# Kernel tuning notes

Hardware: AMD Instinct MI355X
Metric: run time of the kernel (lower is better)

The kernel has to match this reference:

```python
import jax, jax.numpy as jnp
import numpy as np

N_NODES = 100000
N_EDGES = 1600000
IN_DIM, HID_DIM, OUT_DIM = 128, 128, 64


def gcn_conv(x, W, b, src, dst, edge_weight, n_nodes):
    """PyG GCNConv: symmetric norm with self-loops (weight 1.0), x@W, scatter-add, +bias."""
    xw = x @ W                                   # [N, out]
    deg = jax.ops.segment_sum(edge_weight, dst, num_segments=n_nodes) + 1.0  # self-loop weight 1
    dis = jnp.where(deg > 0, jax.lax.rsqrt(deg), 0.0)       # deg^{-1/2}
    norm = dis[src] * edge_weight * dis[dst]                # per-edge norm
    agg = jax.ops.segment_sum(norm[:, None] * xw[src], dst, num_segments=n_nodes)
    self_term = (dis * dis)[:, None] * xw                   # self-loop contribution
    return agg + self_term + b


def setup_inputs() -> dict:
    key = jax.random.key(0)
    ks = jax.random.split(key, 12)
    x = jax.random.normal(ks[0], (N_NODES, IN_DIM), dtype=jnp.float32)
    edge_index = jax.random.randint(ks[1], (2, N_EDGES), 0, N_NODES, dtype=jnp.int64 if jax.config.jax_enable_x64 else jnp.int32)
    edge_curvature = jax.random.normal(ks[2], (N_EDGES, 1), dtype=jnp.float32)
    s = 0.1
    W1 = jax.random.normal(ks[3], (IN_DIM, HID_DIM), dtype=jnp.float32) * s
    b1 = jnp.zeros((HID_DIM,), dtype=jnp.float32)
    W2 = jax.random.normal(ks[4], (HID_DIM, OUT_DIM), dtype=jnp.float32) * s
    b2 = jnp.zeros((OUT_DIM,), dtype=jnp.float32)
    mw1 = jax.random.normal(ks[5], (1, 16), dtype=jnp.float32) * s
    mb1 = jnp.zeros((16,), dtype=jnp.float32)
    mw2 = jax.random.normal(ks[6], (16, 1), dtype=jnp.float32) * s
    mb2 = jnp.zeros((1,), dtype=jnp.float32)
    return {"x": x, "edge_index": edge_index, "edge_curvature": edge_curvature,
            "W1": W1, "b1": b1, "W2": W2, "b2": b2,
            "mw1": mw1, "mb1": mb1, "mw2": mw2, "mb2": mb2}


def reference(x, edge_index, edge_curvature, W1, b1, W2, b2, mw1, mb1, mw2, mb2):
    src, dst = edge_index[0], edge_index[1]
    # curv_mlp: Linear(1,16) -> ReLU -> Linear(16,1) -> Sigmoid
    h = jax.nn.relu(edge_curvature @ mw1 + mb1)
    w = jax.nn.sigmoid(h @ mw2 + mb2)[:, 0]
    edge_weight = 0.1 + 0.9 * w
    h1 = jax.nn.relu(gcn_conv(x, W1, b1, src, dst, edge_weight, N_NODES))
    # dropout p=0.5 is identity in eval mode
    out = gcn_conv(h1, W2, b2, src, dst, edge_weight, N_NODES)
    return out
```

## Files before the change

### kernel.cpp

```cpp
#include <hip/hip_runtime.h>


constexpr int N_NODES = 100000;
constexpr int N_EDGES = 1600000;
constexpr int IN_DIM  = 128;
constexpr int HID_DIM = 128;
constexpr int OUT_DIM = 64;

constexpr int RANGE = 256;
constexpr int NBUK  = (N_NODES + RANGE - 1) / RANGE;
constexpr int EPB   = 4096;
constexpr int NPART = (N_EDGES + EPB - 1) / EPB;

using bf16x8 = __attribute__((ext_vector_type(8))) short;
using f32x4  = __attribute__((ext_vector_type(4))) float;

__device__ __forceinline__ unsigned short f2b(float f)
{
    unsigned int u = __float_as_uint(f);
    u += 0x7fffu + ((u >> 16) & 1u);
    return (unsigned short)(u >> 16);
}

__device__ __forceinline__ float edge_weight_mlp(float c,
                                                 const float* __restrict__ mw1,
                                                 const float* __restrict__ mb1,
                                                 const float* __restrict__ mw2,
                                                 const float* __restrict__ mb2)
{
    float z = mb2[0];
#pragma unroll
    for (int i = 0; i < 16; ++i) {
        float h = fmaf(c, mw1[i], mb1[i]);
        h = fmaxf(h, 0.0f);
        z = fmaf(h, mw2[i], z);
    }
    float s = 1.0f / (1.0f + __expf(-z));
    return fmaf(0.9f, s, 0.1f);
}

__global__ __launch_bounds__(512) void k_hist(const int* __restrict__ dst,
                                              int* __restrict__ blockHist,
                                              int* __restrict__ gcnt)
{
    __shared__ int hist[NBUK];
    const int tid = threadIdx.x;
    for (int i = tid; i < NBUK; i += 512) hist[i] = 0;
    __syncthreads();
    const int base = blockIdx.x * EPB;
    const int n = min(EPB, N_EDGES - base);
    for (int i = tid; i < n; i += 512)
        atomicAdd(&hist[dst[base + i] >> 8], 1);
    __syncthreads();
    for (int i = tid; i < NBUK; i += 512) {
        int h = hist[i];
        blockHist[(size_t)blockIdx.x * NBUK + i] = h;
        if (h) atomicAdd(&gcnt[i], h);
    }
}

__global__ __launch_bounds__(512) void k_scan_buckets(const int* __restrict__ gcnt,
                                                      int* __restrict__ bucketBase)
{
    __shared__ int sm[512];
    const int t = threadIdx.x;
    int v = (t < NBUK) ? gcnt[t] : 0;
    sm[t] = v;
    __syncthreads();
#pragma unroll
    for (int o = 1; o < 512; o <<= 1) {
        int u = (t >= o) ? sm[t - o] : 0;
        __syncthreads();
        sm[t] += u;
        __syncthreads();
    }
    if (t < NBUK) bucketBase[t] = sm[t] - v;
    if (t == NBUK - 1) bucketBase[NBUK] = sm[t];
}

__global__ __launch_bounds__(256) void k_colscan(int* __restrict__ blockHist,
                                                 const int* __restrict__ bucketBase)
{
    int j = blockIdx.x * blockDim.x + threadIdx.x;
    if (j >= NBUK) return;
    int run = bucketBase[j];
    for (int b = 0; b < NPART; ++b) {
        size_t idx = (size_t)b * NBUK + j;
        int t = blockHist[idx];
        blockHist[idx] = run;
        run += t;
    }
}

__global__ __launch_bounds__(512) void k_partition(const float* __restrict__ curv,
                                                   const int*   __restrict__ src,
                                                   const int*   __restrict__ dst,
                                                   const float* __restrict__ mw1,
                                                   const float* __restrict__ mb1,
                                                   const float* __restrict__ mw2,
                                                   const float* __restrict__ mb2,
                                                   const int*   __restrict__ blockHist,
                                                   int2* __restrict__ ep_tmp)
{
    __shared__ int cur[NBUK];
    const int tid = threadIdx.x;
    for (int i = tid; i < NBUK; i += 512)
        cur[i] = blockHist[(size_t)blockIdx.x * NBUK + i];
    __syncthreads();
    const int base = blockIdx.x * EPB;
    const int n = min(EPB, N_EDGES - base);
    for (int i = tid; i < n; i += 512) {
        int e = base + i;
        int d = dst[e];
        float w = edge_weight_mlp(curv[e], mw1, mb1, mw2, mb2);
        int pos = atomicAdd(&cur[d >> 8], 1);
        int meta = src[e] | ((d & (RANGE - 1)) << 17);
        ep_tmp[pos] = make_int2(meta, __float_as_int(w));
    }
}

__global__ __launch_bounds__(256) void k_bucket_sort(const int2* __restrict__ ep_tmp,
                                                     const int*  __restrict__ bucketBase,
                                                     int2* __restrict__ ep,
                                                     int*  __restrict__ rp,
                                                     float* __restrict__ dis)
{
    const int b   = blockIdx.x;
    const int tid = threadIdx.x;
    const int base  = bucketBase[b];
    const int nE    = bucketBase[b + 1] - base;
    const int node0 = b * RANGE;
    const int nNodes = min(RANGE, N_NODES - node0);

    __shared__ int   cnt[RANGE];
    __shared__ float deg[RANGE];
    __shared__ int   sm[RANGE];
    __shared__ int   cur[RANGE];

    cnt[tid] = 0;
    deg[tid] = 0.0f;
    __syncthreads();
    for (int i = tid; i < nE; i += 256) {
        int2 t = ep_tmp[base + i];
        int dl = (t.x >> 17) & (RANGE - 1);
        atomicAdd(&cnt[dl], 1);
        atomicAdd(&deg[dl], __int_as_float(t.y));
    }
    __syncthreads();
    int c = cnt[tid];
    sm[tid] = c;
    __syncthreads();
#pragma unroll
    for (int o = 1; o < 256; o <<= 1) {
        int u = (tid >= o) ? sm[tid - o] : 0;
        __syncthreads();
        sm[tid] += u;
        __syncthreads();
    }
    int excl = sm[tid] - c;
    cur[tid] = base + excl;
    if (tid < nNodes) {
        rp[node0 + tid]  = base + excl;
        dis[node0 + tid] = rsqrtf(deg[tid] + 1.0f);
    }
    if (b == NBUK - 1 && tid == 0) rp[N_NODES] = N_EDGES;
    __syncthreads();
    for (int i = tid; i < nE; i += 256) {
        int2 t = ep_tmp[base + i];
        int dl = (t.x >> 17) & (RANGE - 1);
        int pos = atomicAdd(&cur[dl], 1);
        ep[pos] = make_int2(t.x & 0x1FFFF, t.y);
    }
}

__global__ __launch_bounds__(256) void k_cvt(const float4* __restrict__ in,
                                             uint4* __restrict__ out,
                                             int n8)
{
    int i = blockIdx.x * blockDim.x + threadIdx.x;
    if (i >= n8) return;
    float4 a = in[2 * i];
    float4 b = in[2 * i + 1];
    uint4 o;
    o.x = (unsigned)f2b(a.x) | ((unsigned)f2b(a.y) << 16);
    o.y = (unsigned)f2b(a.z) | ((unsigned)f2b(a.w) << 16);
    o.z = (unsigned)f2b(b.x) | ((unsigned)f2b(b.y) << 16);
    o.w = (unsigned)f2b(b.z) | ((unsigned)f2b(b.w) << 16);
    out[i] = o;
}

template <int KIN, int KOUT>
__global__ __launch_bounds__(256) void k_prepack(const float* __restrict__ W,
                                                 unsigned short* __restrict__ wp)
{
    constexpr int KS = KIN / 32;
    constexpr int NSLOT = (KOUT / 16) * KS * 64;
    int idx = blockIdx.x * blockDim.x + threadIdx.x;
    if (idx >= NSLOT) return;
    int l  = idx & 63;
    int t  = idx >> 6;
    int ks = t % KS;
    int nt = t / KS;
    int col = nt * 16 + (l & 15);
    int k0  = ks * 32 + (l >> 4) * 8;
    unsigned short o[8];
#pragma unroll
    for (int j = 0; j < 8; ++j)
        o[j] = f2b(W[(k0 + j) * KOUT + col]);
    *reinterpret_cast<uint4*>(&wp[(size_t)idx * 8]) = *reinterpret_cast<uint4*>(o);
}

template <int KIN, int KOUT>
__global__ __launch_bounds__(256) void k_gemm_mfma(const unsigned short* __restrict__ Ab,
                                                   const unsigned short* __restrict__ Wp,
                                                   const float* __restrict__ dis,
                                                   unsigned short* __restrict__ C)
{
    constexpr int NT = KOUT / 16;
    constexpr int KS = KIN / 32;
    const int tid  = threadIdx.x;
    const int lane = tid & 63;
    const int wave = blockIdx.x * (blockDim.x >> 6) + (tid >> 6);
    const int row0 = wave * 16;
    if (row0 >= N_NODES) return;

    f32x4 acc[NT];
#pragma unroll
    for (int nt = 0; nt < NT; ++nt)
        acc[nt] = f32x4{0.f, 0.f, 0.f, 0.f};

    const int arow = row0 + (lane & 15);
    const int koff = (lane >> 4) * 8;
#pragma unroll
    for (int ks = 0; ks < KS; ++ks) {
        bf16x8 a = *reinterpret_cast<const bf16x8*>(Ab + (size_t)arow * KIN + ks * 32 + koff);
#pragma unroll
        for (int nt = 0; nt < NT; ++nt) {
            bf16x8 b = *reinterpret_cast<const bf16x8*>(Wp + ((size_t)(nt * KS + ks) * 64 + lane) * 8);
            acc[nt] = __builtin_amdgcn_mfma_f32_16x16x32_bf16(a, b, acc[nt], 0, 0, 0);
        }
    }

    const int r0 = row0 + ((lane >> 4) << 2);
    const int c0 = lane & 15;
    float dv[4];
#pragma unroll
    for (int r = 0; r < 4; ++r) dv[r] = dis[r0 + r];
#pragma unroll
    for (int nt = 0; nt < NT; ++nt) {
#pragma unroll
        for (int r = 0; r < 4; ++r)
            C[(size_t)(r0 + r) * KOUT + nt * 16 + c0] = f2b(acc[nt][r] * dv[r]);
    }
}

template <int DIM, bool RELU, bool OBF16>
__global__ __launch_bounds__(256) void k_gather(const int*  __restrict__ rp,
                                                const int2* __restrict__ ep,
                                                const unsigned short* __restrict__ xws,
                                                const float* __restrict__ dis,
                                                const float* __restrict__ bias,
                                                void* __restrict__ out)
{
    constexpr int TPN = DIM / 8;
    constexpr int NPB = 256 / TPN;
    const int tid = threadIdx.x;
    const int n   = blockIdx.x * NPB + tid / TPN;
    const int d8  = tid % TPN;
    const uint4* xw8 = reinterpret_cast<const uint4*>(xws);
    const int beg = rp[n];
    const int end = rp[n + 1];

    float a0[8] = {0,0,0,0,0,0,0,0};
    float a1[8] = {0,0,0,0,0,0,0,0};

    auto fma8 = [](float w, uint4 u, float* acc) {
        acc[0] = fmaf(w, __uint_as_float(u.x << 16),          acc[0]);
        acc[1] = fmaf(w, __uint_as_float(u.x & 0xFFFF0000u),  acc[1]);
        acc[2] = fmaf(w, __uint_as_float(u.y << 16),          acc[2]);
        acc[3] = fmaf(w, __uint_as_float(u.y & 0xFFFF0000u),  acc[3]);
        acc[4] = fmaf(w, __uint_as_float(u.z << 16),          acc[4]);
        acc[5] = fmaf(w, __uint_as_float(u.z & 0xFFFF0000u),  acc[5]);
        acc[6] = fmaf(w, __uint_as_float(u.w << 16),          acc[6]);
        acc[7] = fmaf(w, __uint_as_float(u.w & 0xFFFF0000u),  acc[7]);
    };

    int i = beg;
    for (; i + 8 <= end; i += 8) {
        int2 e0 = ep[i],     e1 = ep[i + 1], e2 = ep[i + 2], e3 = ep[i + 3];
        int2 e4 = ep[i + 4], e5 = ep[i + 5], e6 = ep[i + 6], e7 = ep[i + 7];
        uint4 u0 = xw8[(size_t)e0.x * TPN + d8];
        uint4 u1 = xw8[(size_t)e1.x * TPN + d8];
        uint4 u2 = xw8[(size_t)e2.x * TPN + d8];
        uint4 u3 = xw8[(size_t)e3.x * TPN + d8];
        uint4 u4 = xw8[(size_t)e4.x * TPN + d8];
        uint4 u5 = xw8[(size_t)e5.x * TPN + d8];
        uint4 u6 = xw8[(size_t)e6.x * TPN + d8];
        uint4 u7 = xw8[(size_t)e7.x * TPN + d8];
        fma8(__int_as_float(e0.y), u0, a0);
        fma8(__int_as_float(e1.y), u1, a1);
        fma8(__int_as_float(e2.y), u2, a0);
        fma8(__int_as_float(e3.y), u3, a1);
        fma8(__int_as_float(e4.y), u4, a0);
        fma8(__int_as_float(e5.y), u5, a1);
        fma8(__int_as_float(e6.y), u6, a0);
        fma8(__int_as_float(e7.y), u7, a1);
    }
    for (; i < end; ++i) {
        int2 e = ep[i];
        uint4 u = xw8[(size_t)e.x * TPN + d8];
        fma8(__int_as_float(e.y), u, a0);
    }
    {
        uint4 un = xw8[(size_t)n * TPN + d8];
        fma8(1.0f, un, a0);
    }

    const float dn = dis[n];
    const float4* b4 = reinterpret_cast<const float4*>(bias);
    float4 blo = b4[d8 * 2];
    float4 bhi = b4[d8 * 2 + 1];
    float v[8];
    v[0] = fmaf(dn, a0[0] + a1[0], blo.x);
    v[1] = fmaf(dn, a0[1] + a1[1], blo.y);
    v[2] = fmaf(dn, a0[2] + a1[2], blo.z);
    v[3] = fmaf(dn, a0[3] + a1[3], blo.w);
    v[4] = fmaf(dn, a0[4] + a1[4], bhi.x);
    v[5] = fmaf(dn, a0[5] + a1[5], bhi.y);
    v[6] = fmaf(dn, a0[6] + a1[6], bhi.z);
    v[7] = fmaf(dn, a0[7] + a1[7], bhi.w);
    if (RELU) {
#pragma unroll
        for (int j = 0; j < 8; ++j) v[j] = fmaxf(v[j], 0.0f);
    }
    if (OBF16) {
        uint4 o;
        o.x = (unsigned)f2b(v[0]) | ((unsigned)f2b(v[1]) << 16);
        o.y = (unsigned)f2b(v[2]) | ((unsigned)f2b(v[3]) << 16);
        o.z = (unsigned)f2b(v[4]) | ((unsigned)f2b(v[5]) << 16);
        o.w = (unsigned)f2b(v[6]) | ((unsigned)f2b(v[7]) << 16);
        reinterpret_cast<uint4*>(out)[(size_t)n * TPN + d8] = o;
    } else {
        float4* o4 = reinterpret_cast<float4*>(out);
        o4[(size_t)n * (DIM / 4) + d8 * 2]     = make_float4(v[0], v[1], v[2], v[3]);
        o4[(size_t)n * (DIM / 4) + d8 * 2 + 1] = make_float4(v[4], v[5], v[6], v[7]);
    }
}

extern "C" void kernel_launch(void* const* d_in, const int* in_sizes, int n_in,
                              void* d_out, int out_size, void* d_ws, size_t ws_size,
                              hipStream_t stream)
{
    const float* x    = (const float*)d_in[0];
    const int*   eidx = (const int*)  d_in[1];
    const float* curv = (const float*)d_in[2];
    const float* W1   = (const float*)d_in[3];
    const float* b1   = (const float*)d_in[4];
    const float* W2   = (const float*)d_in[5];
    const float* b2   = (const float*)d_in[6];
    const float* mw1  = (const float*)d_in[7];
    const float* mb1  = (const float*)d_in[8];
    const float* mw2  = (const float*)d_in[9];
    const float* mb2  = (const float*)d_in[10];

    const int* src = eidx;
    const int* dst = eidx + N_EDGES;
    float* out = (float*)d_out;

    char*  ws  = (char*)d_ws;
    size_t off = 0;
    auto alloc = [&](size_t bytes) -> void* {
        void* p = ws + off;
        off += (bytes + 255) & ~(size_t)255;
        return p;
    };
    float* dis       = (float*)alloc(sizeof(float) * N_NODES);
    int*   rp        = (int*)  alloc(sizeof(int) * (N_NODES + 1));
    int*   gcnt      = (int*)  alloc(sizeof(int) * NBUK);
    int*   bucketBase= (int*)  alloc(sizeof(int) * (NBUK + 1));
    int*   blockHist = (int*)  alloc(sizeof(int) * (size_t)NPART * NBUK);
    int2*  ep_tmp    = (int2*) alloc(sizeof(int2) * N_EDGES);
    int2*  ep        = (int2*) alloc(sizeof(int2) * N_EDGES);
    unsigned short* xb  = (unsigned short*)alloc(sizeof(unsigned short) * (size_t)N_NODES * IN_DIM);
    unsigned short* xws = (unsigned short*)alloc(sizeof(unsigned short) * (size_t)N_NODES * HID_DIM);
    unsigned short* h1b = (unsigned short*)alloc(sizeof(unsigned short) * (size_t)N_NODES * HID_DIM);
    unsigned short* wp1 = (unsigned short*)alloc(sizeof(unsigned short) * (HID_DIM / 16) * (IN_DIM / 32) * 64 * 8);
    unsigned short* wp2 = (unsigned short*)alloc(sizeof(unsigned short) * (OUT_DIM / 16) * (HID_DIM / 32) * 64 * 8);

    hipMemsetAsync(gcnt, 0, sizeof(int) * NBUK, stream);

    const int B = 256;
    auto cdiv = [](long long a, long long b) { return (int)((a + b - 1) / b); };

    k_hist        <<<NPART, 512, 0, stream>>>(dst, blockHist, gcnt);
    k_scan_buckets<<<1, 512, 0, stream>>>(gcnt, bucketBase);
    k_colscan     <<<cdiv(NBUK, B), B, 0, stream>>>(blockHist, bucketBase);
    k_partition   <<<NPART, 512, 0, stream>>>(curv, src, dst, mw1, mb1, mw2, mb2,
                                              blockHist, ep_tmp);
    k_bucket_sort <<<NBUK, 256, 0, stream>>>(ep_tmp, bucketBase, ep, rp, dis);

    k_cvt<<<cdiv((size_t)N_NODES * IN_DIM / 8, B), B, 0, stream>>>(
        (const float4*)x, (uint4*)xb, (int)((size_t)N_NODES * IN_DIM / 8));
    k_prepack<IN_DIM, HID_DIM><<<cdiv((HID_DIM/16)*(IN_DIM/32)*64, B), B, 0, stream>>>(W1, wp1);
    k_prepack<HID_DIM, OUT_DIM><<<cdiv((OUT_DIM/16)*(HID_DIM/32)*64, B), B, 0, stream>>>(W2, wp2);

    const int GEMM_GRID = cdiv(N_NODES / 16, 4);

    k_gemm_mfma<IN_DIM, HID_DIM><<<GEMM_GRID, 256, 0, stream>>>(xb, wp1, dis, xws);
    k_gather<HID_DIM, true, true><<<N_NODES / 16, 256, 0, stream>>>(rp, ep, xws, dis, b1, h1b);

    k_gemm_mfma<HID_DIM, OUT_DIM><<<GEMM_GRID, 256, 0, stream>>>(h1b, wp2, dis, xws);
    k_gather<OUT_DIM, false, false><<<N_NODES / 32, 256, 0, stream>>>(rp, ep, xws, dis, b2, out);
}
```

Before: 228.1 us.

## Fuse fp32-to-bf16 conversion into GEMM, parallelize column scan, stage buckets in LDS

The separate x-to-bf16 conversion kernel is removed, and the first GEMM now reads fp32 x directly and converts in registers. This drops a full write and reread of a 25 MB bf16 copy. The per-block histogram is transposed to bucket-major, and the serial per-column scan becomes a block-parallel LDS scan, with EPB doubled so NPART fits in 256 threads. The bucket sort caches its edges in shared memory so the second pass skips the global reread, at the cost of 48 KB of LDS per block, which may lower occupancy.

Measured after the change: 209.8 us. -8.0%, faster.

```diff
diff --git a/kernel.cpp b/kernel.cpp
--- a/kernel.cpp
+++ b/kernel.cpp
@@ -9,8 +9,9 @@
 
 constexpr int RANGE = 256;
 constexpr int NBUK  = (N_NODES + RANGE - 1) / RANGE;
-constexpr int EPB   = 4096;
+constexpr int EPB   = 8192;
 constexpr int NPART = (N_EDGES + EPB - 1) / EPB;
+constexpr int STAGE_CAP = 6144;
 
 using bf16x8 = __attribute__((ext_vector_type(8))) short;
 using f32x4  = __attribute__((ext_vector_type(4))) float;
@@ -45,16 +46,17 @@
 {
     __shared__ int hist[NBUK];
     const int tid = threadIdx.x;
+    const int b   = blockIdx.x;
     for (int i = tid; i < NBUK; i += 512) hist[i] = 0;
     __syncthreads();
-    const int base = blockIdx.x * EPB;
+    const int base = b * EPB;
     const int n = min(EPB, N_EDGES - base);
     for (int i = tid; i < n; i += 512)
         atomicAdd(&hist[dst[base + i] >> 8], 1);
     __syncthreads();
     for (int i = tid; i < NBUK; i += 512) {
         int h = hist[i];
-        blockHist[(size_t)blockIdx.x * NBUK + i] = h;
+        blockHist[(size_t)i * NPART + b] = h;
         if (h) atomicAdd(&gcnt[i], h);
     }
 }
@@ -81,15 +83,21 @@
 __global__ __launch_bounds__(256) void k_colscan(int* __restrict__ blockHist,
                                                  const int* __restrict__ bucketBase)
 {
-    int j = blockIdx.x * blockDim.x + threadIdx.x;
-    if (j >= NBUK) return;
-    int run = bucketBase[j];
-    for (int b = 0; b < NPART; ++b) {
-        size_t idx = (size_t)b * NBUK + j;
-        int t = blockHist[idx];
-        blockHist[idx] = run;
-        run += t;
-    }
+    const int j = blockIdx.x;
+    const int t = threadIdx.x;
+    __shared__ int sm[256];
+    int v = (t < NPART) ? blockHist[(size_t)j * NPART + t] : 0;
+    sm[t] = v;
+    __syncthreads();
+#pragma unroll
+    for (int o = 1; o < 256; o <<= 1) {
+        int u = (t >= o) ? sm[t - o] : 0;
+        __syncthreads();
+        sm[t] += u;
+        __syncthreads();
+    }
+    if (t < NPART)
+        blockHist[(size_t)j * NPART + t] = bucketBase[j] + sm[t] - v;
 }
 
 __global__ __launch_bounds__(512) void k_partition(const float* __restrict__ curv,
@@ -104,10 +112,11 @@
 {
     __shared__ int cur[NBUK];
     const int tid = threadIdx.x;
+    const int b   = blockIdx.x;
     for (int i = tid; i < NBUK; i += 512)
-        cur[i] = blockHist[(size_t)blockIdx.x * NBUK + i];
-    __syncthreads();
-    const int base = blockIdx.x * EPB;
+        cur[i] = blockHist[(size_t)i * NPART + b];
+    __syncthreads();
+    const int base = b * EPB;
     const int n = min(EPB, N_EDGES - base);
     for (int i = tid; i < n; i += 512) {
         int e = base + i;
@@ -132,16 +141,20 @@
     const int node0 = b * RANGE;
     const int nNodes = min(RANGE, N_NODES - node0);
 
+    __shared__ int2  stage[STAGE_CAP];
     __shared__ int   cnt[RANGE];
     __shared__ float deg[RANGE];
     __shared__ int   sm[RANGE];
     __shared__ int   cur[RANGE];
 
+    const bool fit = (nE <= STAGE_CAP);
+
     cnt[tid] = 0;
     deg[tid] = 0.0f;
     __syncthreads();
     for (int i = tid; i < nE; i += 256) {
         int2 t = ep_tmp[base + i];
+        if (fit) stage[i] = t;
         int dl = (t.x >> 17) & (RANGE - 1);
         atomicAdd(&cnt[dl], 1);
         atomicAdd(&deg[dl], __int_as_float(t.y));
@@ -166,27 +179,11 @@
     if (b == NBUK - 1 && tid == 0) rp[N_NODES] = N_EDGES;
     __syncthreads();
     for (int i = tid; i < nE; i += 256) {
-        int2 t = ep_tmp[base + i];
+        int2 t = fit ? stage[i] : ep_tmp[base + i];
         int dl = (t.x >> 17) & (RANGE - 1);
         int pos = atomicAdd(&cur[dl], 1);
         ep[pos] = make_int2(t.x & 0x1FFFF, t.y);
     }
-}
-
-__global__ __launch_bounds__(256) void k_cvt(const float4* __restrict__ in,
-                                             uint4* __restrict__ out,
-                                             int n8)
-{
-    int i = blockIdx.x * blockDim.x + threadIdx.x;
-    if (i >= n8) return;
-    float4 a = in[2 * i];
-    float4 b = in[2 * i + 1];
-    uint4 o;
-    o.x = (unsigned)f2b(a.x) | ((unsigned)f2b(a.y) << 16);
-    o.y = (unsigned)f2b(a.z) | ((unsigned)f2b(a.w) << 16);
-    o.z = (unsigned)f2b(b.x) | ((unsigned)f2b(b.y) << 16);
-    o.w = (unsigned)f2b(b.z) | ((unsigned)f2b(b.w) << 16);
-    out[i] = o;
 }
 
 template <int KIN, int KOUT>
@@ -210,8 +207,8 @@
     *reinterpret_cast<uint4*>(&wp[(size_t)idx * 8]) = *reinterpret_cast<uint4*>(o);
 }
 
-template <int KIN, int KOUT>
-__global__ __launch_bounds__(256) void k_gemm_mfma(const unsigned short* __restrict__ Ab,
+template <int KIN, int KOUT, bool AFP32>
+__global__ __launch_bounds__(256) void k_gemm_mfma(const void* __restrict__ Aptr,
                                                    const unsigned short* __restrict__ Wp,
                                                    const float* __restrict__ dis,
                                                    unsigned short* __restrict__ C)
@@ -233,11 +230,24 @@
     const int koff = (lane >> 4) * 8;
 #pragma unroll
     for (int ks = 0; ks < KS; ++ks) {
-        bf16x8 a = *reinterpret_cast<const bf16x8*>(Ab + (size_t)arow * KIN + ks * 32 + koff);
+        bf16x8 a;
+        if constexpr (AFP32) {
+            const float* A = (const float*)Aptr;
+            const float* p = A + (size_t)arow * KIN + ks * 32 + koff;
+            float4 f0 = *reinterpret_cast<const float4*>(p);
+            float4 f1 = *reinterpret_cast<const float4*>(p + 4);
+            a[0] = (short)f2b(f0.x); a[1] = (short)f2b(f0.y);
+            a[2] = (short)f2b(f0.z); a[3] = (short)f2b(f0.w);
+            a[4] = (short)f2b(f1.x); a[5] = (short)f2b(f1.y);
+            a[6] = (short)f2b(f1.z); a[7] = (short)f2b(f1.w);
+        } else {
+            const unsigned short* A = (const unsigned short*)Aptr;
+            a = *reinterpret_cast<const bf16x8*>(A + (size_t)arow * KIN + ks * 32 + koff);
+        }
 #pragma unroll
         for (int nt = 0; nt < NT; ++nt) {
-            bf16x8 b = *reinterpret_cast<const bf16x8*>(Wp + ((size_t)(nt * KS + ks) * 64 + lane) * 8);
-            acc[nt] = __builtin_amdgcn_mfma_f32_16x16x32_bf16(a, b, acc[nt], 0, 0, 0);
+            bf16x8 bfr = *reinterpret_cast<const bf16x8*>(Wp + ((size_t)(nt * KS + ks) * 64 + lane) * 8);
+            acc[nt] = __builtin_amdgcn_mfma_f32_16x16x32_bf16(a, bfr, acc[nt], 0, 0, 0);
         }
     }
 
@@ -378,10 +388,9 @@
     int*   rp        = (int*)  alloc(sizeof(int) * (N_NODES + 1));
     int*   gcnt      = (int*)  alloc(sizeof(int) * NBUK);
     int*   bucketBase= (int*)  alloc(sizeof(int) * (NBUK + 1));
-    int*   blockHist = (int*)  alloc(sizeof(int) * (size_t)NPART * NBUK);
+    int*   blockHist = (int*)  alloc(sizeof(int) * (size_t)NBUK * NPART);
     int2*  ep_tmp    = (int2*) alloc(sizeof(int2) * N_EDGES);
     int2*  ep        = (int2*) alloc(sizeof(int2) * N_EDGES);
-    unsigned short* xb  = (unsigned short*)alloc(sizeof(unsigned short) * (size_t)N_NODES * IN_DIM);
     unsigned short* xws = (unsigned short*)alloc(sizeof(unsigned short) * (size_t)N_NODES * HID_DIM);
     unsigned short* h1b = (unsigned short*)alloc(sizeof(unsigned short) * (size_t)N_NODES * HID_DIM);
     unsigned short* wp1 = (unsigned short*)alloc(sizeof(unsigned short) * (HID_DIM / 16) * (IN_DIM / 32) * 64 * 8);
@@ -394,21 +403,19 @@
 
     k_hist        <<<NPART, 512, 0, stream>>>(dst, blockHist, gcnt);
     k_scan_buckets<<<1, 512, 0, stream>>>(gcnt, bucketBase);
-    k_colscan     <<<cdiv(NBUK, B), B, 0, stream>>>(blockHist, bucketBase);
+    k_colscan     <<<NBUK, 256, 0, stream>>>(blockHist, bucketBase);
     k_partition   <<<NPART, 512, 0, stream>>>(curv, src, dst, mw1, mb1, mw2, mb2,
                                               blockHist, ep_tmp);
     k_bucket_sort <<<NBUK, 256, 0, stream>>>(ep_tmp, bucketBase, ep, rp, dis);
 
-    k_cvt<<<cdiv((size_t)N_NODES * IN_DIM / 8, B), B, 0, stream>>>(
-        (const float4*)x, (uint4*)xb, (int)((size_t)N_NODES * IN_DIM / 8));
     k_prepack<IN_DIM, HID_DIM><<<cdiv((HID_DIM/16)*(IN_DIM/32)*64, B), B, 0, stream>>>(W1, wp1);
     k_prepack<HID_DIM, OUT_DIM><<<cdiv((OUT_DIM/16)*(HID_DIM/32)*64, B), B, 0, stream>>>(W2, wp2);
 
     const int GEMM_GRID = cdiv(N_NODES / 16, 4);
 
-    k_gemm_mfma<IN_DIM, HID_DIM><<<GEMM_GRID, 256, 0, stream>>>(xb, wp1, dis, xws);
+    k_gemm_mfma<IN_DIM, HID_DIM, true><<<GEMM_GRID, 256, 0, stream>>>(x, wp1, dis, xws);
     k_gather<HID_DIM, true, true><<<N_NODES / 16, 256, 0, stream>>>(rp, ep, xws, dis, b1, h1b);
 
-    k_gemm_mfma<HID_DIM, OUT_DIM><<<GEMM_GRID, 256, 0, stream>>>(h1b, wp2, dis, xws);
+    k_gemm_mfma<HID_DIM, OUT_DIM, false><<<GEMM_GRID, 256, 0, stream>>>(h1b, wp2, dis, xws);
     k_gather<OUT_DIM, false, false><<<N_NODES / 32, 256, 0, stream>>>(rp, ep, xws, dis, b2, out);
 }
```
